# Kernel optimization log

Measured on AMD Instinct MI355X. Metric: run time of the kernel, lower is better.

## Reference

```python
import jax, jax.numpy as jnp
import numpy as np

K = 3          # kernel_size
PAD = K // 2   # padding applied before deform conv


def setup_inputs() -> dict:
    key = jax.random.key(0)
    ks = jax.random.split(key, 5)
    B, C, H, W = 4, 64, 64, 256
    O = 64  # out_channels
    x = jax.random.normal(ks[0], (B, C, H, W), jnp.float32)
    # offset conv params (torch Conv2d default init scale ~ 1/sqrt(fan_in) ~ 0.04)
    offset_w = jax.random.normal(ks[1], (2 * K * K, C, K, K), jnp.float32) * 0.04
    offset_b = jax.random.normal(ks[2], (2 * K * K,), jnp.float32) * 0.04
    # original module uses torch.rand (uniform [0,1)) for weight and mask
    weight = jax.random.uniform(ks[3], (O, C, K, K), jnp.float32)
    mask = jax.random.uniform(ks[4], (B, K * K, H, W), jnp.float32)
    return dict(x=x, offset_w=offset_w, offset_b=offset_b, weight=weight, mask=mask)


def _trianglewave(x):
    n = jnp.floor(x / np.pi + 0.5)
    sign = 1.0 - 2.0 * jnp.mod(n, 2.0)  # (-1)**n for integer-valued float n
    return (x - np.pi * n) * sign


def prak(x):
    # preluconst = 1.0
    return _trianglewave(x) + _trianglewave(x + np.pi / 2)


def deform_conv2d(xp, offsets, weight, mask):
    # xp: [B,C,Hp,Wp] padded input; offsets: [B,2*K*K,H,W]; weight: [O,C,K,K]; mask: [B,K*K,H,W]
    B, C, Hp, Wp = xp.shape
    H, W = offsets.shape[2], offsets.shape[3]
    P = K * K
    off = offsets.reshape(B, P, 2, H, W)
    off_y, off_x = off[:, :, 0], off[:, :, 1]
    ii = (jnp.arange(P) // K).astype(jnp.float32)  # kernel row per tap p
    jj = (jnp.arange(P) % K).astype(jnp.float32)   # kernel col per tap p
    base_y = jnp.arange(H, dtype=jnp.float32)[None, :, None] + ii[:, None, None]  # [P,H,1]
    base_x = jnp.arange(W, dtype=jnp.float32)[None, None, :] + jj[:, None, None]  # [P,1,W]
    py = base_y[None] + off_y  # [B,P,H,W] sampling rows (stride=1, no extra pad)
    px = base_x[None] + off_x
    y0 = jnp.floor(py)
    x0 = jnp.floor(px)
    flat = xp.reshape(B, C, Hp * Wp)

    def gather(yc, xc):
        valid = (yc >= 0) & (yc <= Hp - 1) & (xc >= 0) & (xc <= Wp - 1)
        yi = jnp.clip(yc, 0, Hp - 1).astype(jnp.int32)
        xi = jnp.clip(xc, 0, Wp - 1).astype(jnp.int32)
        idx = (yi * Wp + xi).reshape(B, 1, -1)  # [B,1,P*H*W]
        v = jnp.take_along_axis(flat, jnp.broadcast_to(idx, (B, C, idx.shape[-1])), axis=2)
        return v.reshape(B, C, P, H, W) * valid.astype(xp.dtype).reshape(B, 1, P, H, W)

    wy1 = py - y0
    wx1 = px - x0
    wy0 = 1.0 - wy1
    wx0 = 1.0 - wx1
    val = (gather(y0, x0) * (wy0 * wx0)[:, None]
           + gather(y0, x0 + 1) * (wy0 * wx1)[:, None]
           + gather(y0 + 1, x0) * (wy1 * wx0)[:, None]
           + gather(y0 + 1, x0 + 1) * (wy1 * wx1)[:, None])  # [B,C,P,H,W]
    val = val * mask[:, None]  # modulation mask
    O = weight.shape[0]
    return jnp.einsum('ocp,bcphw->bohw', weight.reshape(O, C, P), val)


def reference(x, offset_w, offset_b, weight, mask):
    # x: [B,C,H,W]
    x_addon = jax.lax.stop_gradient(x)  # x.detach() branch
    xp = jnp.pad(x, ((0, 0), (0, 0), (PAD, PAD), (PAD, PAD)))
    offsets = jax.lax.conv_general_dilated(
        xp, offset_w, (1, 1), 'VALID',
        dimension_numbers=('NCHW', 'OIHW', 'NCHW')) + offset_b[None, :, None, None]
    y = deform_conv2d(xp, offsets, weight, mask)  # [B,O,H,W]
    # F.layer_norm with normalized_shape == full tensor shape: global mean/var, no affine
    mu = jnp.mean(y)
    var = jnp.mean((y - mu) ** 2)
    y = (y - mu) * jax.lax.rsqrt(var + 1e-5)
    y = prak(y)
    y = jnp.concatenate([y, x_addon], axis=1)  # [B,O+C,H,W]
    # MaxPool2d(kernel_size=K, stride=2), VALID padding
    out = jax.lax.reduce_window(y, -jnp.inf, jax.lax.max,
                                (1, 1, K, K), (1, 1, 2, 2), 'VALID')
    return out
```

## Files before the change

### kernel.cpp

```cpp
#include <hip/hip_runtime.h>
#include <math.h>

#define BN 4
#define CN 64
#define HN 64
#define WN 256
#define ON 64
#define NOC 18
#define PN 9
#define HO 31
#define WO 127

#define VST 584
#define VSB 1168

typedef __attribute__((ext_vector_type(8))) short bf16x8;
typedef __attribute__((ext_vector_type(4))) float f32x4;

__device__ __forceinline__ unsigned short f2bf(float f) {
    unsigned int u = __float_as_uint(f);
    unsigned int r = (u + 0x7fffu + ((u >> 16) & 1u)) >> 16;
    return (unsigned short)r;
}

__device__ __forceinline__ unsigned int cvtpk(float lo, float hi) {
    unsigned int r;
    asm("v_cvt_pk_bf16_f32 %0, %1, %2" : "=v"(r) : "v"(lo), "v"(hi));
    return r;
}

__device__ __forceinline__ float trianglewave(float x) {
    const float PI_F = 3.14159274101257324f;
    float n = floorf(x / PI_F + 0.5f);
    float m = fmodf(n, 2.0f);
    if (m < 0.0f) m += 2.0f;
    float sgn = 1.0f - 2.0f * m;
    return (x - PI_F * n) * sgn;
}

__device__ __forceinline__ float prak_f(float x) {
    const float PI_HALF = 1.57079637050628662f;
    return trianglewave(x) + trianglewave(x + PI_HALF);
}

__global__ __launch_bounds__(512) void prep_transpose_kernel(
        const float* __restrict__ x,
        const float* __restrict__ offw,
        const float* __restrict__ wgt,
        unsigned short* __restrict__ xt,
        unsigned short* __restrict__ Wf,
        unsigned short* __restrict__ WoF) {
    if (blockIdx.x < 512) {
        __shared__ float Tl[128][65];
        int blk = blockIdx.x;
        int whalf = blk & 1;
        int h = (blk >> 1) & 63;
        int b = blk >> 7;
        int t = threadIdx.x;
        int fq = t & 31;
#pragma unroll
        for (int j = 0; j < 4; j++) {
            int c = (t >> 5) + 16 * j;
            float4 v = *(const float4*)(x + ((size_t)(b * CN + c) * HN + h) * WN + whalf * 128 + fq * 4);
            Tl[fq * 4 + 0][c] = v.x;
            Tl[fq * 4 + 1][c] = v.y;
            Tl[fq * 4 + 2][c] = v.z;
            Tl[fq * 4 + 3][c] = v.w;
        }
        __syncthreads();
        int cq = t & 7;
#pragma unroll
        for (int j = 0; j < 2; j++) {
            int wl = (t >> 3) + 64 * j;
            uint4 pk;
            pk.x = cvtpk(Tl[wl][cq * 8 + 0], Tl[wl][cq * 8 + 1]);
            pk.y = cvtpk(Tl[wl][cq * 8 + 2], Tl[wl][cq * 8 + 3]);
            pk.z = cvtpk(Tl[wl][cq * 8 + 4], Tl[wl][cq * 8 + 5]);
            pk.w = cvtpk(Tl[wl][cq * 8 + 6], Tl[wl][cq * 8 + 7]);
            *(uint4*)(xt + (((size_t)(b * HN) + h) * WN + whalf * 128 + wl) * 64 + cq * 8) = pk;
        }
    } else {
        int t = (blockIdx.x - 512) * 512 + threadIdx.x;
        if (t < 4 * 18 * 64 * 8) {
            int j    = t & 7;
            int lane = (t >> 3) & 63;
            int rest = t >> 9;
            int ks   = rest % 18;
            int m    = rest / 18;
            int o = m * 16 + (lane & 15);
            int k = ks * 32 + (lane >> 4) * 8 + j;
            int c = k & 63;
            int p = k >> 6;
            Wf[t] = f2bf(wgt[(o * CN + c) * 9 + p]);
        }
        if (t < 2 * 18 * 64 * 8) {
            int j    = t & 7;
            int lane = (t >> 3) & 63;
            int rest = t >> 9;
            int ks   = rest % 18;
            int mo   = rest / 18;
            int o = mo * 16 + (lane & 15);
            int k = ks * 32 + (lane >> 4) * 8 + j;
            int c = k & 63;
            int p = k >> 6;
            WoF[t] = (o < NOC) ? f2bf(offw[(o * CN + c) * 9 + p]) : (unsigned short)0;
        }
    }
}

struct TapS { float w00, w01, w10, w11; int a0, a1, a2, a3; };

__global__ __launch_bounds__(512, 4) void fused_kernel(
        const unsigned short* __restrict__ xt,
        const float* __restrict__ offb,
        const float* __restrict__ mask,
        const unsigned short* __restrict__ WoF,
        const unsigned short* __restrict__ Wf,
        float* __restrict__ y,
        float2* __restrict__ partials) {
    __shared__ __align__(16) unsigned short V[64 * VST];
    __shared__ float offs_lds[NOC * 64];
    __shared__ float red1[8], red2[8];

    int bid = blockIdx.x;
    int logical = ((bid & 7) << 7) + (bid >> 3);
    int b = logical >> 8;
    int h = (logical >> 2) & 63;
    int wblk = logical & 3;
    int lane = threadIdx.x & 63;
    int wv = threadIdx.x >> 6;

    int pl = threadIdx.x >> 3;
    int cg = threadIdx.x & 7;
    int w = (wblk << 6) + pl;
    const unsigned short* xb = xt + (size_t)b * HN * WN * 64;
    const uint4* xb4 = (const uint4*)xb;
    int kq = lane >> 4;

#pragma unroll
    for (int p = 0; p < PN; p++) {
        int iy = h + p / 3 - 1;
        int ix = w + p % 3 - 1;
        uint4 pk = {0u, 0u, 0u, 0u};
        if (iy >= 0 && iy < HN && ix >= 0 && ix < WN)
            pk = xb4[((size_t)iy * WN + ix) * 8 + cg];
        *(uint4*)((char*)V + pl * VSB + p * 128 + cg * 16) = pk;
    }
    __syncthreads();

    {
        int mo = wv >> 2;
        int nt = wv & 3;
        f32x4 acc = {0.0f, 0.0f, 0.0f, 0.0f};
        const bf16x8* Wov = (const bf16x8*)WoF;
        int pixc = nt * 16 + (lane & 15);
#pragma unroll
        for (int ks = 0; ks < 18; ks++) {
            bf16x8 a = Wov[(mo * 18 + ks) * 64 + lane];
            bf16x8 bfr = *(const bf16x8*)((char*)V + pixc * VSB + ks * 64 + kq * 16);
            acc = __builtin_amdgcn_mfma_f32_16x16x32_bf16(a, bfr, acc, 0, 0, 0);
        }
        int ocb = mo * 16 + kq * 4;
#pragma unroll
        for (int r = 0; r < 4; r++) {
            int oc = ocb + r;
            if (oc < NOC) offs_lds[oc * 64 + pixc] = acc[r] + offb[oc];
        }
    }
    __syncthreads();

    {
        float mkv[9];
#pragma unroll
        for (int p = 0; p < 9; p++) mkv[p] = mask[((b * PN + p) * HN + h) * WN + w];

        auto stage = [&](int p) -> TapS {
            TapS s;
            float offy = offs_lds[(2 * p) * 64 + pl];
            float offx = offs_lds[(2 * p + 1) * 64 + pl];
            float mk = mkv[p];
            float py = (float)(h + p / 3) + offy;
            float px = (float)(w + p % 3) + offx;
            float fy0 = floorf(py), fx0 = floorf(px);
            float wy1 = py - fy0, wx1 = px - fx0;
            float wy0 = 1.0f - wy1, wx0 = 1.0f - wx1;
            int iy0 = (int)fy0 - 1, ix0 = (int)fx0 - 1;
            int iy1 = iy0 + 1, ix1 = ix0 + 1;
            bool vy0 = (iy0 >= 0) && (iy0 < HN);
            bool vy1 = (iy1 >= 0) && (iy1 < HN);
            bool vx0 = (ix0 >= 0) && (ix0 < WN);
            bool vx1 = (ix1 >= 0) && (ix1 < WN);
            s.w00 = (vy0 && vx0) ? wy0 * wx0 * mk : 0.0f;
            s.w01 = (vy0 && vx1) ? wy0 * wx1 * mk : 0.0f;
            s.w10 = (vy1 && vx0) ? wy1 * wx0 * mk : 0.0f;
            s.w11 = (vy1 && vx1) ? wy1 * wx1 * mk : 0.0f;
            int cy0 = min(max(iy0, 0), HN - 1), cy1 = min(max(iy1, 0), HN - 1);
            int cx0 = min(max(ix0, 0), WN - 1), cx1 = min(max(ix1, 0), WN - 1);
            s.a0 = (cy0 * WN + cx0) * 8 + cg;
            s.a1 = (cy0 * WN + cx1) * 8 + cg;
            s.a2 = (cy1 * WN + cx0) * 8 + cg;
            s.a3 = (cy1 * WN + cx1) * 8 + cg;
            return s;
        };

        TapS sC = stage(0);
        uint4 A = xb4[sC.a0], B = xb4[sC.a1], C = xb4[sC.a2], D = xb4[sC.a3];

#pragma unroll
        for (int p = 0; p < 9; p++) {
            TapS sN;
            uint4 nA, nB, nC, nD;
            if (p < 8) {
                sN = stage(p + 1);
                nA = xb4[sN.a0]; nB = xb4[sN.a1];
                nC = xb4[sN.a2]; nD = xb4[sN.a3];
            }
            float fa[8], fb[8], fc[8], fd[8];
            {
                unsigned int ua[4] = {A.x, A.y, A.z, A.w};
                unsigned int ub[4] = {B.x, B.y, B.z, B.w};
                unsigned int uc[4] = {C.x, C.y, C.z, C.w};
                unsigned int ud[4] = {D.x, D.y, D.z, D.w};
#pragma unroll
                for (int j = 0; j < 4; j++) {
                    fa[2 * j] = __uint_as_float(ua[j] << 16);
                    fa[2 * j + 1] = __uint_as_float(ua[j] & 0xffff0000u);
                    fb[2 * j] = __uint_as_float(ub[j] << 16);
                    fb[2 * j + 1] = __uint_as_float(ub[j] & 0xffff0000u);
                    fc[2 * j] = __uint_as_float(uc[j] << 16);
                    fc[2 * j + 1] = __uint_as_float(uc[j] & 0xffff0000u);
                    fd[2 * j] = __uint_as_float(ud[j] << 16);
                    fd[2 * j + 1] = __uint_as_float(ud[j] & 0xffff0000u);
                }
            }
            float v[8];
#pragma unroll
            for (int j = 0; j < 8; j++)
                v[j] = sC.w00 * fa[j] + sC.w01 * fb[j] + sC.w10 * fc[j] + sC.w11 * fd[j];
            uint4 pk;
            pk.x = cvtpk(v[0], v[1]);
            pk.y = cvtpk(v[2], v[3]);
            pk.z = cvtpk(v[4], v[5]);
            pk.w = cvtpk(v[6], v[7]);
            *(uint4*)((char*)V + pl * VSB + p * 128 + cg * 16) = pk;
            if (p < 8) {
                sC = sN;
                A = nA; B = nB; C = nC; D = nD;
            }
        }
    }
    __syncthreads();

    int m = wv >> 1;
    int npair = wv & 1;
    f32x4 acc0 = {0.0f, 0.0f, 0.0f, 0.0f};
    f32x4 acc1 = {0.0f, 0.0f, 0.0f, 0.0f};
    const bf16x8* Wfv = (const bf16x8*)Wf;
    int pixc = npair * 32 + (lane & 15);
#pragma unroll
    for (int ks = 0; ks < 18; ks++) {
        bf16x8 a  = Wfv[(m * 18 + ks) * 64 + lane];
        bf16x8 b0 = *(const bf16x8*)((char*)V + pixc * VSB + ks * 64 + kq * 16);
        bf16x8 b1 = *(const bf16x8*)((char*)V + (pixc + 16) * VSB + ks * 64 + kq * 16);
        acc0 = __builtin_amdgcn_mfma_f32_16x16x32_bf16(a, b0, acc0, 0, 0, 0);
        acc1 = __builtin_amdgcn_mfma_f32_16x16x32_bf16(a, b1, acc1, 0, 0, 0);
    }

    int orow = m * 16 + kq * 4;
    float s1 = 0.0f, s2 = 0.0f;
#pragma unroll
    for (int r = 0; r < 4; r++) {
        float v0 = acc0[r];
        float v1 = acc1[r];
        size_t base = (((size_t)(b * ON + orow + r) * HN) + h) * WN + (wblk << 6);
        y[base + pixc] = v0;
        y[base + pixc + 16] = v1;
        s1 += v0 + v1;
        s2 += v0 * v0 + v1 * v1;
    }
#pragma unroll
    for (int off = 32; off > 0; off >>= 1) {
        s1 += __shfl_down(s1, off);
        s2 += __shfl_down(s2, off);
    }
    if (lane == 0) { red1[wv] = s1; red2[wv] = s2; }
    __syncthreads();
    if (threadIdx.x == 0) {
        float t1 = 0.0f, t2 = 0.0f;
#pragma unroll
        for (int i = 0; i < 8; i++) { t1 += red1[i]; t2 += red2[i]; }
        partials[blockIdx.x] = make_float2(t1, t2);
    }
}

__global__ __launch_bounds__(256) void stats_kernel(const float2* __restrict__ partials,
                                                    int nblocks,
                                                    float* __restrict__ stats) {
    __shared__ double r1[256], r2[256];
    int tid = threadIdx.x;
    double s1 = 0.0, s2 = 0.0;
    for (int i = tid; i < nblocks; i += 256) {
        s1 += (double)partials[i].x;
        s2 += (double)partials[i].y;
    }
    r1[tid] = s1;
    r2[tid] = s2;
    __syncthreads();
    for (int s = 128; s > 0; s >>= 1) {
        if (tid < s) { r1[tid] += r1[tid + s]; r2[tid] += r2[tid + s]; }
        __syncthreads();
    }
    if (tid == 0) {
        double N = (double)BN * ON * HN * WN;
        double mu = r1[0] / N;
        double var = r2[0] / N - mu * mu;
        stats[0] = (float)mu;
        stats[1] = (float)(1.0 / sqrt(var + 1e-5));
    }
}

__global__ __launch_bounds__(256) void out_kernel(const float* __restrict__ yb,
                                                  const float* __restrict__ x,
                                                  const float* __restrict__ stats,
                                                  float* __restrict__ out) {
    int t = blockIdx.x * 256 + threadIdx.x;
    int q  = t & 31;
    int r  = t >> 5;
    int oh = r % 31;
    int cr = r / 31;
    int ch = cr & 127;
    int b  = cr >> 7;

    float mu = stats[0];
    float inv = stats[1];
    float m0 = -INFINITY, m1 = -INFINITY, m2 = -INFINITY, m3 = -INFINITY;
    const float* plane = (ch < 64)
        ? yb + ((size_t)(b * ON + ch) * HN) * WN
        : x + ((size_t)(b * CN + (ch - 64)) * HN) * WN;
    bool doPrak = (ch < 64);

#pragma unroll
    for (int dy = 0; dy < 3; dy++) {
        const float* row = plane + (2 * oh + dy) * WN + 8 * q;
        float2 r0 = *(const float2*)(row + 0);
        float2 r1 = *(const float2*)(row + 2);
        float2 r2 = *(const float2*)(row + 4);
        float2 r3 = *(const float2*)(row + 6);
        float  e8 = row[8];
        float e[9] = {r0.x, r0.y, r1.x, r1.y, r2.x, r2.y, r3.x, r3.y, e8};
        if (doPrak) {
#pragma unroll
            for (int i = 0; i < 9; i++) e[i] = prak_f((e[i] - mu) * inv);
        }
        m0 = fmaxf(m0, fmaxf(fmaxf(e[0], e[1]), e[2]));
        m1 = fmaxf(m1, fmaxf(fmaxf(e[2], e[3]), e[4]));
        m2 = fmaxf(m2, fmaxf(fmaxf(e[4], e[5]), e[6]));
        m3 = fmaxf(m3, fmaxf(fmaxf(e[6], e[7]), e[8]));
    }

    int ow0 = q * 4;
    size_t obase = (((size_t)(b * 128 + ch) * HO) + oh) * WO + ow0;
    out[obase + 0] = m0;
    out[obase + 1] = m1;
    out[obase + 2] = m2;
    if (ow0 + 3 < WO) out[obase + 3] = m3;
}

extern "C" void kernel_launch(void* const* d_in, const int* in_sizes, int n_in,
                              void* d_out, int out_size, void* d_ws, size_t ws_size,
                              hipStream_t stream) {
    const float* x    = (const float*)d_in[0];
    const float* offw = (const float*)d_in[1];
    const float* offb = (const float*)d_in[2];
    const float* wgt  = (const float*)d_in[3];
    const float* mask = (const float*)d_in[4];
    float* out = (float*)d_out;

    unsigned short* Wf  = (unsigned short*)d_ws;
    unsigned short* WoF = Wf + 36864;
    float* y  = (float*)(WoF + 18432);
    unsigned short* xt = (unsigned short*)(y + 4194304);
    float2* partials = (float2*)(xt + 4194304);
    float* stats = (float*)(partials + 1024);

    prep_transpose_kernel<<<584, 512, 0, stream>>>(x, offw, wgt, xt, Wf, WoF);
    fused_kernel<<<1024, 512, 0, stream>>>(xt, offb, mask, WoF, Wf, y, partials);
    stats_kernel<<<1, 256, 0, stream>>>(partials, 1024, stats);
    out_kernel<<<1984, 256, 0, stream>>>(y, x, stats, out);
}
```

Before: 58.95 us.

## Load offset-conv B fragments directly from global and fold stats into out_kernel

The offset-convolution MFMA now reads its bf16 B fragments straight from the transposed input in global memory. This drops the LDS staging pass and the barrier that followed it. Separately, the single-block stats kernel is removed, and every out_kernel block redundantly reduces the 1024 partial sums in double precision to get the mean and inverse std. This saves one launch and its serialization, at the cost of repeated reduction work per block and more uncoalesced global loads in the MFMA loop.

```diff
diff --git a/kernel.cpp b/kernel.cpp
--- a/kernel.cpp
+++ b/kernel.cpp
@@ -137,27 +137,24 @@
     const uint4* xb4 = (const uint4*)xb;
     int kq = lane >> 4;
 
-#pragma unroll
-    for (int p = 0; p < PN; p++) {
-        int iy = h + p / 3 - 1;
-        int ix = w + p % 3 - 1;
-        uint4 pk = {0u, 0u, 0u, 0u};
-        if (iy >= 0 && iy < HN && ix >= 0 && ix < WN)
-            pk = xb4[((size_t)iy * WN + ix) * 8 + cg];
-        *(uint4*)((char*)V + pl * VSB + p * 128 + cg * 16) = pk;
-    }
-    __syncthreads();
-
     {
         int mo = wv >> 2;
         int nt = wv & 3;
         f32x4 acc = {0.0f, 0.0f, 0.0f, 0.0f};
         const bf16x8* Wov = (const bf16x8*)WoF;
         int pixc = nt * 16 + (lane & 15);
+        int wg = (wblk << 6) + pixc;
 #pragma unroll
         for (int ks = 0; ks < 18; ks++) {
+            int kbase = ks * 32 + kq * 8;
+            int p = kbase >> 6;
+            int coff = kbase & 63;
+            int iy = h + p / 3 - 1;
+            int ix = wg + p % 3 - 1;
+            bf16x8 bfr = {0, 0, 0, 0, 0, 0, 0, 0};
+            if (iy >= 0 && iy < HN && ix >= 0 && ix < WN)
+                bfr = *(const bf16x8*)(xb + ((size_t)iy * WN + ix) * 64 + coff);
             bf16x8 a = Wov[(mo * 18 + ks) * 64 + lane];
-            bf16x8 bfr = *(const bf16x8*)((char*)V + pixc * VSB + ks * 64 + kq * 16);
             acc = __builtin_amdgcn_mfma_f32_16x16x32_bf16(a, bfr, acc, 0, 0, 0);
         }
         int ocb = mo * 16 + kq * 4;
@@ -293,37 +290,39 @@
     }
 }
 
-__global__ __launch_bounds__(256) void stats_kernel(const float2* __restrict__ partials,
-                                                    int nblocks,
-                                                    float* __restrict__ stats) {
-    __shared__ double r1[256], r2[256];
-    int tid = threadIdx.x;
-    double s1 = 0.0, s2 = 0.0;
-    for (int i = tid; i < nblocks; i += 256) {
-        s1 += (double)partials[i].x;
-        s2 += (double)partials[i].y;
-    }
-    r1[tid] = s1;
-    r2[tid] = s2;
-    __syncthreads();
-    for (int s = 128; s > 0; s >>= 1) {
-        if (tid < s) { r1[tid] += r1[tid + s]; r2[tid] += r2[tid + s]; }
-        __syncthreads();
-    }
-    if (tid == 0) {
-        double N = (double)BN * ON * HN * WN;
-        double mu = r1[0] / N;
-        double var = r2[0] / N - mu * mu;
-        stats[0] = (float)mu;
-        stats[1] = (float)(1.0 / sqrt(var + 1e-5));
-    }
-}
-
 __global__ __launch_bounds__(256) void out_kernel(const float* __restrict__ yb,
                                                   const float* __restrict__ x,
-                                                  const float* __restrict__ stats,
+                                                  const float2* __restrict__ partials,
                                                   float* __restrict__ out) {
-    int t = blockIdx.x * 256 + threadIdx.x;
+    __shared__ double r1[256], r2[256];
+    __shared__ float sstats[2];
+    int tid = threadIdx.x;
+    {
+        double s1 = 0.0, s2 = 0.0;
+        for (int i = tid; i < 1024; i += 256) {
+            s1 += (double)partials[i].x;
+            s2 += (double)partials[i].y;
+        }
+        r1[tid] = s1;
+        r2[tid] = s2;
+        __syncthreads();
+        for (int s = 128; s > 0; s >>= 1) {
+            if (tid < s) { r1[tid] += r1[tid + s]; r2[tid] += r2[tid + s]; }
+            __syncthreads();
+        }
+        if (tid == 0) {
+            double N = (double)BN * ON * HN * WN;
+            double mu = r1[0] / N;
+            double var = r2[0] / N - mu * mu;
+            sstats[0] = (float)mu;
+            sstats[1] = (float)(1.0 / sqrt(var + 1e-5));
+        }
+        __syncthreads();
+    }
+    float mu = sstats[0];
+    float inv = sstats[1];
+
+    int t = blockIdx.x * 256 + tid;
     int q  = t & 31;
     int r  = t >> 5;
     int oh = r % 31;
@@ -331,8 +330,6 @@
     int ch = cr & 127;
     int b  = cr >> 7;
 
-    float mu = stats[0];
-    float inv = stats[1];
     float m0 = -INFINITY, m1 = -INFINITY, m2 = -INFINITY, m3 = -INFINITY;
     const float* plane = (ch < 64)
         ? yb + ((size_t)(b * ON + ch) * HN) * WN
@@ -343,11 +340,11 @@
     for (int dy = 0; dy < 3; dy++) {
         const float* row = plane + (2 * oh + dy) * WN + 8 * q;
         float2 r0 = *(const float2*)(row + 0);
-        float2 r1 = *(const float2*)(row + 2);
-        float2 r2 = *(const float2*)(row + 4);
-        float2 r3 = *(const float2*)(row + 6);
+        float2 r1v = *(const float2*)(row + 2);
+        float2 r2v = *(const float2*)(row + 4);
+        float2 r3v = *(const float2*)(row + 6);
         float  e8 = row[8];
-        float e[9] = {r0.x, r0.y, r1.x, r1.y, r2.x, r2.y, r3.x, r3.y, e8};
+        float e[9] = {r0.x, r0.y, r1v.x, r1v.y, r2v.x, r2v.y, r3v.x, r3v.y, e8};
         if (doPrak) {
 #pragma unroll
             for (int i = 0; i < 9; i++) e[i] = prak_f((e[i] - mu) * inv);
@@ -381,10 +378,8 @@
     float* y  = (float*)(WoF + 18432);
     unsigned short* xt = (unsigned short*)(y + 4194304);
     float2* partials = (float2*)(xt + 4194304);
-    float* stats = (float*)(partials + 1024);
 
     prep_transpose_kernel<<<584, 512, 0, stream>>>(x, offw, wgt, xt, Wf, WoF);
     fused_kernel<<<1024, 512, 0, stream>>>(xt, offb, mask, WoF, Wf, y, partials);
-    stats_kernel<<<1, 256, 0, stream>>>(partials, 1024, stats);
-    out_kernel<<<1984, 256, 0, stream>>>(y, x, stats, out);
-}
+    out_kernel<<<1984, 256, 0, stream>>>(y, x, partials, out);
+}
```

Measured after the change: 68.60 us. 16.4% more time.
